# Performance work log

Hardware: AMD Instinct MI355X
Metric: run time of the kernel (lower is better)

Reference implementation:

```python
import jax, jax.numpy as jnp
import numpy as np

HEADS = 8


def pe_table(length, d):
    # standard sinusoidal positional encoding [length, d]
    pos = jnp.arange(length, dtype=jnp.float32)[:, None]
    div = jnp.exp(jnp.arange(0, d, 2, dtype=jnp.float32) * (-np.log(10000.0) / d))
    ang = pos * div
    pe = jnp.zeros((length, d), jnp.float32)
    pe = pe.at[:, 0::2].set(jnp.sin(ang)).at[:, 1::2].set(jnp.cos(ang))
    return pe


def layernorm(x, a, b, eps=1e-6):
    mu = x.mean(-1, keepdims=True)
    sd = jnp.std(x, axis=-1, ddof=1, keepdims=True)  # torch .std() is unbiased
    return a * (x - mu) / (sd + eps) + b


def setup_inputs() -> dict:
    key = jax.random.key(0)
    ks = jax.random.split(key, 16)
    B, N, T, L = 8, 8, 512, 512
    ts_c, ts_e = 64, 192
    aux_c, aux_e = 16, 64
    edge_c = 8
    d = 256
    s = 0.02
    w = lambda k, shape: jax.random.normal(k, shape, jnp.float32) * s
    return {
        'x': jax.random.normal(ks[0], (B, T, d), jnp.float32),
        'nbr_ts': jax.random.normal(ks[1], (B, N, ts_c, L), jnp.float32),
        'nbr_aux': jax.random.normal(ks[2], (B, N, aux_c, L), jnp.float32),
        'nbr_edge': jax.random.normal(ks[3], (B, N, edge_c, T), jnp.float32),
        'attn_mask': jax.random.randint(ks[4], (B, N, 1, L), 0, 2).astype(jnp.int32),
        'Wts': w(ks[5], (ts_e, ts_c)), 'bts': jnp.zeros((ts_e,), jnp.float32),
        'Waux': w(ks[6], (aux_e, aux_c)), 'baux': jnp.zeros((aux_e,), jnp.float32),
        'Wedge': w(ks[7], (d, edge_c)), 'bedge': jnp.zeros((d,), jnp.float32),
        'ln_a': jnp.ones((d,), jnp.float32), 'ln_b': jnp.zeros((d,), jnp.float32),
        'Wq': w(ks[8], (d, d)), 'bq': jnp.zeros((d,), jnp.float32),
        'Wk': w(ks[9], (d, d)), 'bk': jnp.zeros((d,), jnp.float32),
        'Wv': w(ks[10], (d, d)), 'bv': jnp.zeros((d,), jnp.float32),
        'Wo': w(ks[11], (d, d)), 'bo': jnp.zeros((d,), jnp.float32),
    }


def reference(x, nbr_ts, nbr_aux, nbr_edge, attn_mask,
              Wts, bts, Waux, baux, Wedge, bedge, ln_a, ln_b,
              Wq, bq, Wk, bk, Wv, bv, Wo, bo):
    B, T, d = x.shape
    N, L = nbr_ts.shape[1], nbr_ts.shape[-1]
    h = HEADS
    dk = d // h

    x_pe = x + pe_table(T, d)                                   # [B,T,d]

    # per-neighbor projections (transpose channel-first inputs, then Linear)
    ts_emb = jnp.einsum('bncl,ec->bnle', nbr_ts, Wts) + bts     # [B,N,L,ts_e]
    aux_emb = jnp.einsum('bncl,ec->bnle', nbr_aux, Waux) + baux # [B,N,L,aux_e]
    kv = jnp.concatenate([ts_emb, aux_emb], axis=-1)            # [B,N,L,d]
    kv = kv + pe_table(L, d)

    # SublayerConnection: x + cross_attn(norm(x), kv, kv, mask)
    q_in = layernorm(x_pe, ln_a, ln_b)
    q = (q_in @ Wq.T + bq).reshape(B, T, h, dk).transpose(0, 2, 1, 3)  # [B,h,T,dk]
    k = (kv @ Wk.T + bk).reshape(B, N, L, h, dk)
    v = (kv @ Wv.T + bv).reshape(B, N, L, h, dk)

    scores = jnp.einsum('bhtd,bnlhd->bnhtl', q, k) / jnp.sqrt(jnp.float32(dk))
    mask = attn_mask[:, :, None, :, :]                          # [B,N,1,1,L]
    scores = jnp.where(mask == 0, jnp.float32(-1e9), scores)
    p = jax.nn.softmax(scores, axis=-1)
    ctx = jnp.einsum('bnhtl,bnlhd->bnthd', p, v).reshape(B, N, T, d)
    attn = ctx @ Wo.T + bo                                      # [B,N,T,d]

    sub_out = x_pe[:, None, :, :] + attn                        # residual, [B,N,T,d]

    edge = jnp.einsum('bnct,dc->bntd', nbr_edge, Wedge) + bedge # [B,N,T,d]
    return (sub_out * edge).mean(axis=1)                        # mean over neighbors
```

## Files before the change

### kernel.cpp

```cpp
#include <hip/hip_runtime.h>
#include <hip/hip_bf16.h>
#include <math.h>

typedef __attribute__((ext_vector_type(8))) short bf16x8;
typedef __attribute__((ext_vector_type(4))) short bf16x4;
typedef __attribute__((ext_vector_type(4))) float f32x4;

__device__ __forceinline__ short f2bf(float f) {
    return (short)__builtin_bit_cast(unsigned short, __float2bfloat16(f));
}
__device__ __forceinline__ float bf2f(short s) {
    return __builtin_bit_cast(float, ((unsigned)(unsigned short)s) << 16);
}
__device__ __forceinline__ unsigned pk2bf(float a, float b) {
    return ((unsigned)(unsigned short)f2bf(b) << 16) |
           (unsigned)(unsigned short)f2bf(a);
}

#if defined(__has_builtin)
#if __has_builtin(__builtin_amdgcn_mfma_f32_16x16x16bf16_1k)
#define HAVE_MFMA16 1
#endif
#endif

__device__ __forceinline__ f32x4 mfma16(bf16x4 a, bf16x4 b, f32x4 c) {
#ifdef HAVE_MFMA16
    return __builtin_amdgcn_mfma_f32_16x16x16bf16_1k(a, b, c, 0, 0, 0);
#else
    f32x4 d;
    asm volatile("v_mfma_f32_16x16x16_bf16 %0, %1, %2, %3"
                 : "=v"(d) : "v"(a), "v"(b), "v"(c));
    return d;
#endif
}

#define SCALE2 0.25503482403f

__global__ __launch_bounds__(512) void setup_kernel(
    const float* __restrict__ Wq, const float* __restrict__ Wk,
    const float* __restrict__ Wv, const float* __restrict__ Wo,
    const float* __restrict__ Wts, const float* __restrict__ Waux,
    const float* __restrict__ bts, const float* __restrict__ baux,
    const float* __restrict__ bk, const float* __restrict__ bv,
    const float* __restrict__ x, const float* __restrict__ ln_a,
    const float* __restrict__ ln_b, const int* __restrict__ mask,
    short* __restrict__ wout, short* __restrict__ W2,
    float* __restrict__ bias2, float* __restrict__ bkv,
    float* __restrict__ pe, int* __restrict__ pos, int* __restrict__ cnt,
    short* __restrict__ xpe_bf, short* __restrict__ qin) {
    __shared__ float redA[8];
    __shared__ float redB[8];
    __shared__ int wsum[8];
    int bid = blockIdx.x, tid = threadIdx.x;
    if (bid < 128) {
        int i = bid * 512 + tid;
        wout[i]          = f2bf(Wq[i]);
        wout[65536 + i]  = f2bf(Wk[i]);
        wout[131072 + i] = f2bf(Wv[i]);
        wout[196608 + i] = f2bf(Wo[i]);
    } else if (bid < 176) {
        int idx = (bid - 128) * 512 + tid;
        int e = idx / 96, ch = idx - e * 96;
        float v = 0.f;
        if (ch < 64) { if (e < 192) v = Wts[e * 64 + ch]; }
        else if (ch < 80) { if (e >= 192) v = Waux[(e - 192) * 16 + (ch - 64)]; }
        W2[idx] = f2bf(v);
        if (idx < 256) bias2[idx] = idx < 192 ? bts[idx] : baux[idx - 192];
        if (idx < 512) bkv[idx] = idx < 256 ? bk[idx] : bv[idx - 256];
    } else if (bid < 432) {
        int t = (bid - 176) * 2 + (tid >> 8);
        int dd = tid & 255;
        int i = dd >> 1;
        float div = expf((float)(2 * i) * (-9.210340371976184f / 256.0f));
        float ang = (float)t * div;
        pe[t * 256 + dd] = (dd & 1) ? cosf(ang) : sinf(ang);
    } else if (bid < 496) {
        int bn = bid - 432;
        int lane = tid & 63, wid = tid >> 6;
        int m = mask[bn * 512 + tid] != 0;
        int v = m;
#pragma unroll
        for (int off = 1; off < 64; off <<= 1) {
            int t = __shfl_up(v, off);
            if (lane >= off) v += t;
        }
        if (lane == 63) wsum[wid] = v;
        __syncthreads();
        int base = 0;
#pragma unroll
        for (int w = 0; w < 8; ++w) base += (w < wid) ? wsum[w] : 0;
        pos[bn * 512 + tid] = m ? (base + v - 1) : -1;
        if (tid == 511) cnt[bn] = base + v;
    } else {
        int half = tid >> 8;
        int d = tid & 255;
        int row = (bid - 496) * 2 + half;
        int t = row & 511;
        int i = d >> 1;
        float div = expf((float)(2 * i) * (-9.210340371976184f / 256.0f));
        float ang = (float)t * div;
        float pev = (d & 1) ? cosf(ang) : sinf(ang);
        float v = x[(size_t)row * 256 + d] + pev;
        xpe_bf[(size_t)row * 256 + d] = f2bf(v);
        float s = v;
#pragma unroll
        for (int off = 32; off > 0; off >>= 1) s += __shfl_xor(s, off);
        if ((tid & 63) == 0) redA[tid >> 6] = s;
        __syncthreads();
        int rb = half * 4;
        float mu = (redA[rb] + redA[rb + 1] + redA[rb + 2] + redA[rb + 3]) *
                   (1.0f / 256.0f);
        float dv = v - mu;
        float s2 = dv * dv;
#pragma unroll
        for (int off = 32; off > 0; off >>= 1) s2 += __shfl_xor(s2, off);
        if ((tid & 63) == 0) redB[tid >> 6] = s2;
        __syncthreads();
        float var = (redB[rb] + redB[rb + 1] + redB[rb + 2] + redB[rb + 3]) *
                    (1.0f / 255.0f);
        float sd = sqrtf(var);
        qin[(size_t)row * 256 + d] = f2bf(ln_a[d] * dv / (sd + 1e-6f) + ln_b[d]);
    }
}

__global__ __launch_bounds__(512, 2) void kv_gemm(
    const float* __restrict__ nbr_ts, const float* __restrict__ nbr_aux,
    const short* __restrict__ W2, const float* __restrict__ bias2,
    const float* __restrict__ pe, const int* __restrict__ pos,
    short* __restrict__ kvc) {
    __shared__ __align__(16) float S1[64 * 132];
    __shared__ __align__(16) float S2[16 * 132];
    __shared__ __align__(16) short A_lds[128 * 104];
    int tid = threadIdx.x;
    int bn = blockIdx.x, l0 = blockIdx.y * 128;
    const float* tsb = nbr_ts + (size_t)bn * 64 * 512;
    const float* axb = nbr_aux + (size_t)bn * 16 * 512;
#pragma unroll
    for (int it = 0; it < 4; ++it) {
        int idx = tid + it * 512;
        int cc = idx >> 5, lq = idx & 31;
        *(float4*)&S1[cc * 132 + lq * 4] =
            *(const float4*)&tsb[(size_t)cc * 512 + l0 + lq * 4];
    }
    {
        int cc = tid >> 5, lq = tid & 31;
        *(float4*)&S2[cc * 132 + lq * 4] =
            *(const float4*)&axb[(size_t)cc * 512 + l0 + lq * 4];
    }
    __syncthreads();
#pragma unroll
    for (int p = 0; p < 3; ++p) {
        int tk = tid + p * 512;
        int l = tk & 127, chunk = tk >> 7;
        union { bf16x8 v; unsigned u[4]; } v8;
        if (chunk < 8) {
#pragma unroll
            for (int i = 0; i < 4; ++i)
                v8.u[i] = pk2bf(S1[(chunk * 8 + 2 * i) * 132 + l],
                                S1[(chunk * 8 + 2 * i + 1) * 132 + l]);
        } else if (chunk < 10) {
#pragma unroll
            for (int i = 0; i < 4; ++i)
                v8.u[i] = pk2bf(S2[((chunk - 8) * 8 + 2 * i) * 132 + l],
                                S2[((chunk - 8) * 8 + 2 * i + 1) * 132 + l]);
        } else {
#pragma unroll
            for (int i = 0; i < 4; ++i) v8.u[i] = 0;
        }
        *(bf16x8*)&A_lds[l * 104 + chunk * 8] = v8.v;
    }
    __syncthreads();
    int wid = tid >> 6, lane = tid & 63;
    int g = lane >> 4, c = lane & 15;
    int lm = wid >> 2, le = wid & 3;
    bf16x8 wf[4][3];
#pragma unroll
    for (int nf = 0; nf < 4; ++nf)
#pragma unroll
        for (int ks = 0; ks < 3; ++ks)
            wf[nf][ks] = *(const bf16x8*)&W2[(size_t)(le * 64 + nf * 16 + c) * 96 +
                                             ks * 32 + g * 8];
    f32x4 acc[4][4];
#pragma unroll
    for (int i = 0; i < 4; ++i)
#pragma unroll
        for (int j = 0; j < 4; ++j) acc[i][j] = (f32x4){0.f, 0.f, 0.f, 0.f};
#pragma unroll
    for (int ks = 0; ks < 3; ++ks) {
#pragma unroll
        for (int mf = 0; mf < 4; ++mf) {
            bf16x8 af = *(const bf16x8*)&A_lds[(lm * 64 + mf * 16 + c) * 104 +
                                               ks * 32 + g * 8];
#pragma unroll
            for (int nf = 0; nf < 4; ++nf)
                acc[mf][nf] = __builtin_amdgcn_mfma_f32_16x16x32_bf16(
                    af, wf[nf][ks], acc[mf][nf], 0, 0, 0);
        }
    }
    float b2c[4];
#pragma unroll
    for (int nf = 0; nf < 4; ++nf) b2c[nf] = bias2[le * 64 + nf * 16 + c];
    short* kvb = kvc + (size_t)bn * 512 * 256;
    const int* posb = pos + bn * 512 + l0;
#pragma unroll
    for (int mf = 0; mf < 4; ++mf) {
#pragma unroll
        for (int r = 0; r < 4; ++r) {
            int lr = lm * 64 + mf * 16 + g * 4 + r;
            int p = posb[lr];
            if (p >= 0) {
#pragma unroll
                for (int nf = 0; nf < 4; ++nf) {
                    int e = le * 64 + nf * 16 + c;
                    kvb[(size_t)p * 256 + e] =
                        f2bf(acc[mf][nf][r] + b2c[nf] +
                             pe[(size_t)(l0 + lr) * 256 + e]);
                }
            }
        }
    }
}

__global__ __launch_bounds__(256) void proj_gemm(
    const short* __restrict__ qin, const short* __restrict__ kvc,
    const short* __restrict__ wq, const short* __restrict__ wkv,
    const float* __restrict__ bq, const float* __restrict__ bkv,
    const int* __restrict__ cnt, short* __restrict__ qout,
    short* __restrict__ kv2) {
    int bx = blockIdx.x;
    const short* A; const short* Wm; const float* bias; short* C;
    int row0, col0, LDC; float esc;
    if (bx < 64) {
        row0 = (bx >> 1) * 128; col0 = (bx & 1) * 128;
        A = qin; Wm = wq; bias = bq; C = qout; LDC = 256; esc = SCALE2;
    } else {
        int idx = bx - 64;
        int bn = idx >> 4, mt = (idx >> 2) & 3, ct = idx & 3;
        int nvp = (cnt[bn] + 15) & ~15;
        row0 = mt * 128;
        if (row0 >= nvp) return;
        col0 = ct * 128;
        A = kvc + (size_t)bn * 512 * 256; Wm = wkv; bias = bkv;
        C = kv2 + (size_t)bn * 512 * 512; LDC = 512; esc = 1.0f;
    }
    __shared__ __align__(16) short As[128 * 40];
    __shared__ __align__(16) short Bs[128 * 40];
    int tid = threadIdx.x;
    int wid = tid >> 6, lane = tid & 63;
    int wm = wid >> 1, wn = wid & 1;
    int g = lane >> 4, c = lane & 15;
    f32x4 acc[4][4];
#pragma unroll
    for (int i = 0; i < 4; ++i)
#pragma unroll
        for (int j = 0; j < 4; ++j) acc[i][j] = (f32x4){0.f, 0.f, 0.f, 0.f};

    for (int k0 = 0; k0 < 256; k0 += 32) {
#pragma unroll
        for (int it = 0; it < 2; ++it) {
            int idx = tid + it * 256;
            int r = idx >> 2, ch = idx & 3;
            *(bf16x8*)&As[r * 40 + ch * 8] =
                *(const bf16x8*)&A[(size_t)(row0 + r) * 256 + k0 + ch * 8];
            *(bf16x8*)&Bs[r * 40 + ch * 8] =
                *(const bf16x8*)&Wm[(size_t)(col0 + r) * 256 + k0 + ch * 8];
        }
        __syncthreads();
        bf16x8 af[4], bfr[4];
#pragma unroll
        for (int mf = 0; mf < 4; ++mf)
            af[mf] = *(const bf16x8*)&As[(wm * 64 + mf * 16 + c) * 40 + g * 8];
#pragma unroll
        for (int nf = 0; nf < 4; ++nf)
            bfr[nf] = *(const bf16x8*)&Bs[(wn * 64 + nf * 16 + c) * 40 + g * 8];
#pragma unroll
        for (int mf = 0; mf < 4; ++mf)
#pragma unroll
            for (int nf = 0; nf < 4; ++nf)
                acc[mf][nf] = __builtin_amdgcn_mfma_f32_16x16x32_bf16(
                    af[mf], bfr[nf], acc[mf][nf], 0, 0, 0);
        __syncthreads();
    }
#pragma unroll
    for (int nf = 0; nf < 4; ++nf) {
        int col = col0 + wn * 64 + nf * 16 + c;
        float bz = bias[col];
#pragma unroll
        for (int mf = 0; mf < 4; ++mf)
#pragma unroll
            for (int r = 0; r < 4; ++r) {
                int row = row0 + wm * 64 + mf * 16 + g * 4 + r;
                C[(size_t)row * LDC + col] = f2bf((acc[mf][nf][r] + bz) * esc);
            }
    }
}

template <bool MASKED>
__device__ __forceinline__ void attn_step(
    const short* K_lds, const short* Vt_lds, const bf16x8* qf,
    f32x4 (*ctxa)[2], f32x4* rsv, int l0, int nv, int g, int c) {
    bf16x8 ak = *(const bf16x8*)&K_lds[(l0 + c) * 40 + g * 8];
    bf16x4 vb0 = *(const bf16x4*)&Vt_lds[c * 524 + l0 + g * 4];
    bf16x4 vb1 = *(const bf16x4*)&Vt_lds[(16 + c) * 524 + l0 + g * 4];
    int lb = l0 + g * 4;
#pragma unroll
    for (int tf = 0; tf < 4; ++tf) {
        f32x4 s = __builtin_amdgcn_mfma_f32_16x16x32_bf16(
            ak, qf[tf], (f32x4){0.f, 0.f, 0.f, 0.f}, 0, 0, 0);
        float p0 = exp2f(s[0]);
        float p1 = exp2f(s[1]);
        float p2 = exp2f(s[2]);
        float p3 = exp2f(s[3]);
        if (MASKED) {
            p0 = (lb + 0 < nv) ? p0 : 0.f;
            p1 = (lb + 1 < nv) ? p1 : 0.f;
            p2 = (lb + 2 < nv) ? p2 : 0.f;
            p3 = (lb + 3 < nv) ? p3 : 0.f;
        }
        rsv[tf] += (f32x4){p0, p1, p2, p3};
        union { bf16x4 v; unsigned u[2]; } pu;
        pu.u[0] = pk2bf(p0, p1);
        pu.u[1] = pk2bf(p2, p3);
        __builtin_amdgcn_s_setprio(1);
        ctxa[tf][0] = mfma16(pu.v, vb0, ctxa[tf][0]);
        ctxa[tf][1] = mfma16(pu.v, vb1, ctxa[tf][1]);
        __builtin_amdgcn_s_setprio(0);
    }
}

__global__ __launch_bounds__(512, 2) void attn_kernel(
    const short* __restrict__ Q, const short* __restrict__ KV2,
    const int* __restrict__ cnt, short* __restrict__ ctx) {
    __shared__ __align__(16) short K_lds[512 * 40];
    __shared__ __align__(16) short Vt_lds[32 * 524];
    int tid = threadIdx.x;
    int bx = blockIdx.x;
    int h = bx & 7, bn = bx >> 3, b = bn >> 3;
    int nv = cnt[bn];
    int nvp = (nv + 15) & ~15;
    const short* kvr = KV2 + (size_t)bn * 512 * 512 + h * 32;
#pragma unroll
    for (int it = 0; it < 4; ++it) {
        int idx = tid + it * 512;
        int i = idx >> 2, ch = idx & 3;
        if (i < nvp) {
            bf16x8 kval = (bf16x8){0, 0, 0, 0, 0, 0, 0, 0};
            bf16x8 vval = (bf16x8){0, 0, 0, 0, 0, 0, 0, 0};
            if (i < nv) {
                kval = *(const bf16x8*)&kvr[(size_t)i * 512 + ch * 8];
                vval = *(const bf16x8*)&kvr[(size_t)i * 512 + 256 + ch * 8];
            }
            *(bf16x8*)&K_lds[i * 40 + ch * 8] = kval;
#pragma unroll
            for (int k = 0; k < 8; ++k)
                Vt_lds[(ch * 8 + k) * 524 + i] = vval[k];
        }
    }
    __syncthreads();

    int wid = tid >> 6, lane = tid & 63;
    int g = lane >> 4, c = lane & 15;
    int t0 = wid * 64;
    const short* qg = Q + ((size_t)b * 512 + t0 + c) * 256 + h * 32 + g * 8;
    bf16x8 qf[4];
#pragma unroll
    for (int tf = 0; tf < 4; ++tf)
        qf[tf] = *(const bf16x8*)&qg[(size_t)tf * 16 * 256];

    f32x4 ctxa[4][2];
    f32x4 rsv[4];
#pragma unroll
    for (int tf = 0; tf < 4; ++tf) {
        ctxa[tf][0] = (f32x4){0.f, 0.f, 0.f, 0.f};
        ctxa[tf][1] = (f32x4){0.f, 0.f, 0.f, 0.f};
        rsv[tf] = (f32x4){0.f, 0.f, 0.f, 0.f};
    }
    int nfull = nv & ~15;
    for (int l0 = 0; l0 < nfull; l0 += 16)
        attn_step<false>(K_lds, Vt_lds, qf, ctxa, rsv, l0, nv, g, c);
    if (nfull < nvp)
        attn_step<true>(K_lds, Vt_lds, qf, ctxa, rsv, nfull, nv, g, c);
#ifndef HAVE_MFMA16
    asm volatile("s_nop 7\ns_nop 7");
#endif
#pragma unroll
    for (int tf = 0; tf < 4; ++tf) {
        float r = (rsv[tf][0] + rsv[tf][1]) + (rsv[tf][2] + rsv[tf][3]);
        r += __shfl_xor(r, 16);
        r += __shfl_xor(r, 32);
        float inv = 1.f / r;
#pragma unroll
        for (int rr = 0; rr < 4; ++rr) {
            float invr = __shfl(inv, (lane & 48) | (g * 4 + rr));
            ctxa[tf][0][rr] *= invr;
            ctxa[tf][1][rr] *= invr;
        }
    }
    __syncthreads();
#pragma unroll
    for (int tf = 0; tf < 4; ++tf)
#pragma unroll
        for (int df = 0; df < 2; ++df)
#pragma unroll
            for (int rr = 0; rr < 4; ++rr)
                K_lds[(t0 + tf * 16 + g * 4 + rr) * 40 + df * 16 + c] =
                    f2bf(ctxa[tf][df][rr]);
    __syncthreads();
    short* cg = ctx + (size_t)bn * 512 * 256 + h * 32;
#pragma unroll
    for (int it = 0; it < 4; ++it) {
        int idx = tid + it * 512;
        int l = idx >> 2, ch = idx & 3;
        *(bf16x8*)&cg[(size_t)l * 256 + ch * 8] =
            *(const bf16x8*)&K_lds[l * 40 + ch * 8];
    }
}

__global__ __launch_bounds__(256, 3) void wo_final(
    const short* __restrict__ ctx, const short* __restrict__ wo,
    const float* __restrict__ bo, const short* __restrict__ xpe,
    const float* __restrict__ nbr_edge, const float* __restrict__ Wedge,
    const float* __restrict__ bedge, float* __restrict__ out) {
    __shared__ __align__(16) short Ws[64 * 264];
    __shared__ __align__(16) short As[32 * 264];
    __shared__ __align__(16) float edge_s[8][36];
    int bx = blockIdx.x;
    int b = bx >> 6, tt = (bx >> 2) & 15, dt = bx & 3;
    int t0 = tt * 32, d0 = dt * 64;
    int tid = threadIdx.x;
    int wid = tid >> 6, lane = tid & 63;
    int th = wid & 1, dh = wid >> 1;
    int g = lane >> 4, c = lane & 15;

#pragma unroll
    for (int it = 0; it < 8; ++it) {
        int idx = tid + it * 256;
        int r = idx >> 5, kk = (idx & 31) * 8;
        *(bf16x8*)&Ws[r * 264 + kk] =
            *(const bf16x8*)&wo[(size_t)(d0 + r) * 256 + kk];
    }
    int trloc = th * 16 + g * 4;
    int dcol[2];
    float we[2][8], be[2], xb[2][4];
#pragma unroll
    for (int j = 0; j < 2; ++j) {
        dcol[j] = d0 + dh * 32 + j * 16 + c;
#pragma unroll
        for (int cc = 0; cc < 8; ++cc) we[j][cc] = Wedge[dcol[j] * 8 + cc];
        be[j] = bedge[dcol[j]];
        float boj = bo[dcol[j]];
#pragma unroll
        for (int r = 0; r < 4; ++r)
            xb[j][r] = bf2f(xpe[((size_t)b * 512 + t0 + trloc + r) * 256 +
                                dcol[j]]) + boj;
    }
    f32x4 oacc[2] = {(f32x4){0.f, 0.f, 0.f, 0.f}, (f32x4){0.f, 0.f, 0.f, 0.f}};

    for (int n = 0; n < 8; ++n) {
        int bn = b * 8 + n;
#pragma unroll
        for (int it = 0; it < 4; ++it) {
            int idx = tid + it * 256;
            int r = idx >> 5, kk = (idx & 31) * 8;
            *(bf16x8*)&As[r * 264 + kk] =
                *(const bf16x8*)&ctx[((size_t)bn * 512 + t0 + r) * 256 + kk];
        }
        {
            int cc = tid >> 5, tl = tid & 31;
            edge_s[cc][tl] = nbr_edge[((size_t)bn * 8 + cc) * 512 + t0 + tl];
        }
        __syncthreads();
        f32x4 acc[2] = {(f32x4){0.f, 0.f, 0.f, 0.f},
                        (f32x4){0.f, 0.f, 0.f, 0.f}};
#pragma unroll
        for (int k0 = 0; k0 < 8; ++k0) {
            bf16x8 af = *(const bf16x8*)&As[(th * 16 + c) * 264 + k0 * 32 + g * 8];
#pragma unroll
            for (int j = 0; j < 2; ++j) {
                bf16x8 bf = *(const bf16x8*)&Ws[(dh * 32 + j * 16 + c) * 264 +
                                                k0 * 32 + g * 8];
                acc[j] = __builtin_amdgcn_mfma_f32_16x16x32_bf16(af, bf, acc[j],
                                                                 0, 0, 0);
            }
        }
#pragma unroll
        for (int j = 0; j < 2; ++j)
#pragma unroll
            for (int r = 0; r < 4; ++r) {
                float e = be[j];
#pragma unroll
                for (int cc = 0; cc < 8; ++cc)
                    e = fmaf(edge_s[cc][trloc + r], we[j][cc], e);
                oacc[j][r] = fmaf(acc[j][r] + xb[j][r], e, oacc[j][r]);
            }
        __syncthreads();
    }
#pragma unroll
    for (int j = 0; j < 2; ++j)
#pragma unroll
        for (int r = 0; r < 4; ++r)
            out[((size_t)b * 512 + t0 + trloc + r) * 256 + dcol[j]] =
                oacc[j][r] * 0.125f;
}

extern "C" void kernel_launch(void* const* d_in, const int* in_sizes, int n_in,
                              void* d_out, int out_size, void* d_ws, size_t ws_size,
                              hipStream_t stream) {
    const float* x        = (const float*)d_in[0];
    const float* nbr_ts   = (const float*)d_in[1];
    const float* nbr_aux  = (const float*)d_in[2];
    const float* nbr_edge = (const float*)d_in[3];
    const int*   mask     = (const int*)d_in[4];
    const float* Wts  = (const float*)d_in[5];
    const float* bts  = (const float*)d_in[6];
    const float* Waux = (const float*)d_in[7];
    const float* baux = (const float*)d_in[8];
    const float* Wedge= (const float*)d_in[9];
    const float* bedge= (const float*)d_in[10];
    const float* ln_a = (const float*)d_in[11];
    const float* ln_b = (const float*)d_in[12];
    const float* Wq = (const float*)d_in[13];
    const float* bq = (const float*)d_in[14];
    const float* Wk = (const float*)d_in[15];
    const float* bk = (const float*)d_in[16];
    const float* Wv = (const float*)d_in[17];
    const float* bv = (const float*)d_in[18];
    const float* Wo = (const float*)d_in[19];
    const float* bo = (const float*)d_in[20];
    float* out = (float*)d_out;

    char* W = (char*)d_ws;
    float* pe_f    = (float*)(W);
    short* xpe_bf  = (short*)(W + 524288);
    short* qin_bf  = (short*)(W + 4718592);
    short* q_bf    = (short*)(W + 6815744);
    short* kvc_bf  = (short*)(W + 8912896);
    short* kv2c_bf = (short*)(W + 25690112);
    short* ctx_bf  = (short*)(W + 59244544);
    short* w_bf    = (short*)(W + 92798976);
    short* W2_bf   = (short*)(W + 93323264);
    float* bias2_f = (float*)(W + 93372416);
    float* bkv_f   = (float*)(W + 93373440);
    int*   pos     = (int*)  (W + 93375488);
    int*   cnt     = (int*)  (W + 93506560);
    short* wq_bf = w_bf;
    short* wkv_bf = w_bf + 65536;
    short* wo_bf = w_bf + 196608;

    setup_kernel<<<2544, 512, 0, stream>>>(
        Wq, Wk, Wv, Wo, Wts, Waux, bts, baux, bk, bv, x, ln_a, ln_b, mask,
        w_bf, W2_bf, bias2_f, bkv_f, pe_f, pos, cnt, xpe_bf, qin_bf);
    kv_gemm<<<dim3(64, 4), 512, 0, stream>>>(nbr_ts, nbr_aux, W2_bf, bias2_f,
                                             pe_f, pos, kvc_bf);
    proj_gemm<<<1088, 256, 0, stream>>>(qin_bf, kvc_bf, wq_bf, wkv_bf, bq,
                                        bkv_f, cnt, q_bf, kv2c_bf);
    attn_kernel<<<512, 512, 0, stream>>>(q_bf, kv2c_bf, cnt, ctx_bf);
    wo_final<<<512, 256, 0, stream>>>(ctx_bf, wo_bf, bo, xpe_bf, nbr_edge,
                                      Wedge, bedge, out);
}
```

Measured before the change: 104.7 us.

## Chunk attention KV staging through a smaller LDS buffer to raise occupancy

Attention now stages K and transposed V through a fixed 352-row LDS buffer and loops over chunks of valid keys, instead of holding all 512 rows at once. The ctx write-back is split into two 256-row passes so it fits in the smaller K buffer. Launch bounds rise from 2 to 6 blocks per CU. The aim is more resident blocks per CU for latency hiding, at the cost of extra barriers when the valid-key count exceeds the buffer size. The tighter launch bound may also force register spills.

```diff
diff --git a/kernel.cpp b/kernel.cpp
--- a/kernel.cpp
+++ b/kernel.cpp
@@ -35,6 +35,8 @@
 }
 
 #define SCALE2 0.25503482403f
+#define CAP 352
+#define VS  (CAP + 12)
 
 __global__ __launch_bounds__(512) void setup_kernel(
     const float* __restrict__ Wq, const float* __restrict__ Wk,
@@ -298,10 +300,10 @@
 template <bool MASKED>
 __device__ __forceinline__ void attn_step(
     const short* K_lds, const short* Vt_lds, const bf16x8* qf,
-    f32x4 (*ctxa)[2], f32x4* rsv, int l0, int nv, int g, int c) {
+    f32x4 (*ctxa)[2], f32x4* rsv, int l0, int clen, int g, int c) {
     bf16x8 ak = *(const bf16x8*)&K_lds[(l0 + c) * 40 + g * 8];
-    bf16x4 vb0 = *(const bf16x4*)&Vt_lds[c * 524 + l0 + g * 4];
-    bf16x4 vb1 = *(const bf16x4*)&Vt_lds[(16 + c) * 524 + l0 + g * 4];
+    bf16x4 vb0 = *(const bf16x4*)&Vt_lds[c * VS + l0 + g * 4];
+    bf16x4 vb1 = *(const bf16x4*)&Vt_lds[(16 + c) * VS + l0 + g * 4];
     int lb = l0 + g * 4;
 #pragma unroll
     for (int tf = 0; tf < 4; ++tf) {
@@ -312,10 +314,10 @@
         float p2 = exp2f(s[2]);
         float p3 = exp2f(s[3]);
         if (MASKED) {
-            p0 = (lb + 0 < nv) ? p0 : 0.f;
-            p1 = (lb + 1 < nv) ? p1 : 0.f;
-            p2 = (lb + 2 < nv) ? p2 : 0.f;
-            p3 = (lb + 3 < nv) ? p3 : 0.f;
+            p0 = (lb + 0 < clen) ? p0 : 0.f;
+            p1 = (lb + 1 < clen) ? p1 : 0.f;
+            p2 = (lb + 2 < clen) ? p2 : 0.f;
+            p3 = (lb + 3 < clen) ? p3 : 0.f;
         }
         rsv[tf] += (f32x4){p0, p1, p2, p3};
         union { bf16x4 v; unsigned u[2]; } pu;
@@ -328,35 +330,16 @@
     }
 }
 
-__global__ __launch_bounds__(512, 2) void attn_kernel(
+__global__ __launch_bounds__(512, 6) void attn_kernel(
     const short* __restrict__ Q, const short* __restrict__ KV2,
     const int* __restrict__ cnt, short* __restrict__ ctx) {
-    __shared__ __align__(16) short K_lds[512 * 40];
-    __shared__ __align__(16) short Vt_lds[32 * 524];
+    __shared__ __align__(16) short K_lds[CAP * 40];
+    __shared__ __align__(16) short Vt_lds[32 * VS];
     int tid = threadIdx.x;
     int bx = blockIdx.x;
     int h = bx & 7, bn = bx >> 3, b = bn >> 3;
     int nv = cnt[bn];
-    int nvp = (nv + 15) & ~15;
     const short* kvr = KV2 + (size_t)bn * 512 * 512 + h * 32;
-#pragma unroll
-    for (int it = 0; it < 4; ++it) {
-        int idx = tid + it * 512;
-        int i = idx >> 2, ch = idx & 3;
-        if (i < nvp) {
-            bf16x8 kval = (bf16x8){0, 0, 0, 0, 0, 0, 0, 0};
-            bf16x8 vval = (bf16x8){0, 0, 0, 0, 0, 0, 0, 0};
-            if (i < nv) {
-                kval = *(const bf16x8*)&kvr[(size_t)i * 512 + ch * 8];
-                vval = *(const bf16x8*)&kvr[(size_t)i * 512 + 256 + ch * 8];
-            }
-            *(bf16x8*)&K_lds[i * 40 + ch * 8] = kval;
-#pragma unroll
-            for (int k = 0; k < 8; ++k)
-                Vt_lds[(ch * 8 + k) * 524 + i] = vval[k];
-        }
-    }
-    __syncthreads();
 
     int wid = tid >> 6, lane = tid & 63;
     int g = lane >> 4, c = lane & 15;
@@ -375,11 +358,33 @@
         ctxa[tf][1] = (f32x4){0.f, 0.f, 0.f, 0.f};
         rsv[tf] = (f32x4){0.f, 0.f, 0.f, 0.f};
     }
-    int nfull = nv & ~15;
-    for (int l0 = 0; l0 < nfull; l0 += 16)
-        attn_step<false>(K_lds, Vt_lds, qf, ctxa, rsv, l0, nv, g, c);
-    if (nfull < nvp)
-        attn_step<true>(K_lds, Vt_lds, qf, ctxa, rsv, nfull, nv, g, c);
+
+    for (int base = 0; base < nv; base += CAP) {
+        int rem = nv - base;
+        int clen = rem < CAP ? rem : CAP;
+        int clenp = (clen + 15) & ~15;
+        if (base) __syncthreads();
+        for (int idx = tid; idx < clenp * 4; idx += 512) {
+            int i = idx >> 2, ch = idx & 3;
+            bf16x8 kval = (bf16x8){0, 0, 0, 0, 0, 0, 0, 0};
+            bf16x8 vval = (bf16x8){0, 0, 0, 0, 0, 0, 0, 0};
+            if (i < clen) {
+                size_t ro = (size_t)(base + i) * 512;
+                kval = *(const bf16x8*)&kvr[ro + ch * 8];
+                vval = *(const bf16x8*)&kvr[ro + 256 + ch * 8];
+            }
+            *(bf16x8*)&K_lds[i * 40 + ch * 8] = kval;
+#pragma unroll
+            for (int k = 0; k < 8; ++k)
+                Vt_lds[(ch * 8 + k) * VS + i] = vval[k];
+        }
+        __syncthreads();
+        int nfull = clen & ~15;
+        for (int l0 = 0; l0 < nfull; l0 += 16)
+            attn_step<false>(K_lds, Vt_lds, qf, ctxa, rsv, l0, clen, g, c);
+        if (nfull < clenp)
+            attn_step<true>(K_lds, Vt_lds, qf, ctxa, rsv, nfull, clen, g, c);
+    }
 #ifndef HAVE_MFMA16
     asm volatile("s_nop 7\ns_nop 7");
 #endif
@@ -397,22 +402,29 @@
         }
     }
     __syncthreads();
-#pragma unroll
-    for (int tf = 0; tf < 4; ++tf)
-#pragma unroll
-        for (int df = 0; df < 2; ++df)
-#pragma unroll
-            for (int rr = 0; rr < 4; ++rr)
-                K_lds[(t0 + tf * 16 + g * 4 + rr) * 40 + df * 16 + c] =
-                    f2bf(ctxa[tf][df][rr]);
-    __syncthreads();
     short* cg = ctx + (size_t)bn * 512 * 256 + h * 32;
 #pragma unroll
-    for (int it = 0; it < 4; ++it) {
-        int idx = tid + it * 512;
-        int l = idx >> 2, ch = idx & 3;
-        *(bf16x8*)&cg[(size_t)l * 256 + ch * 8] =
-            *(const bf16x8*)&K_lds[l * 40 + ch * 8];
+    for (int pass = 0; pass < 2; ++pass) {
+        if ((t0 >> 8) == pass) {
+            int tl = t0 & 255;
+#pragma unroll
+            for (int tf = 0; tf < 4; ++tf)
+#pragma unroll
+                for (int df = 0; df < 2; ++df)
+#pragma unroll
+                    for (int rr = 0; rr < 4; ++rr)
+                        K_lds[(tl + tf * 16 + g * 4 + rr) * 40 + df * 16 + c] =
+                            f2bf(ctxa[tf][df][rr]);
+        }
+        __syncthreads();
+#pragma unroll
+        for (int it = 0; it < 2; ++it) {
+            int idx = tid + it * 512;
+            int l = idx >> 2, ch = idx & 3;
+            *(bf16x8*)&cg[(size_t)(pass * 256 + l) * 256 + ch * 8] =
+                *(const bf16x8*)&K_lds[l * 40 + ch * 8];
+        }
+        if (pass == 0) __syncthreads();
     }
 }
 
```

Result: slower. 109.6 us (+4.6%).
